# Optimization experiments

Hardware: AMD Instinct MI355X
Metric: run time of the kernel (lower is better)

The kernel has to match this reference:

```python
import jax, jax.numpy as jnp
import numpy as np

L = 64            # max_l (spherical harmonic bandlimit)
NLAT = L          # latitude samples (Gauss-Legendre nodes)
NLON = 2 * L - 1  # longitude samples
C_IN = 64
C_OUT = 64
T_EMB = 128


def _legendre(Lmax, x):
    """Normalized associated Legendre Pbar_lm(x) (spherical-harmonic norm,
    Condon-Shortley phase) for m>=0. Returns (Lmax, Lmax, nlat)."""
    sx = np.sqrt(np.maximum(1.0 - x * x, 0.0))
    P = np.zeros((Lmax, Lmax, x.size))
    P[0, 0] = np.sqrt(1.0 / (4.0 * np.pi))
    for m in range(1, Lmax):
        P[m, m] = -np.sqrt((2 * m + 1) / (2.0 * m)) * sx * P[m - 1, m - 1]
    for m in range(Lmax - 1):
        P[m + 1, m] = np.sqrt(2 * m + 3.0) * x * P[m, m]
    for m in range(Lmax):
        for l in range(m + 2, Lmax):
            a = np.sqrt((4.0 * l * l - 1.0) / (l * l - m * m))
            b = np.sqrt(((l - 1.0) ** 2 - m * m) / (4.0 * (l - 1.0) ** 2 - 1.0))
            P[l, m] = a * (x * P[l - 1, m] - b * P[l - 2, m])
    return P


def _sht_matrices():
    # Gauss-Legendre quadrature in cos(theta): exact SHT for bandlimited signals
    xg, wg = np.polynomial.legendre.leggauss(NLAT)
    P = _legendre(L, xg)
    # extend to negative m: Pbar_{l,-m} = (-1)^m Pbar_{l,m}; m index offset L-1 (s2fft layout)
    Pfull = np.zeros((L, 2 * L - 1, NLAT))
    Pfull[:, L - 1] = P[:, 0]
    for m in range(1, L):
        Pfull[:, L - 1 + m] = P[:, m]
        Pfull[:, L - 1 - m] = ((-1) ** m) * P[:, m]
    m_idx = np.arange(-(L - 1), L) % NLON  # FFT bin for each m (bijective since NLON=2L-1)
    return jnp.asarray(Pfull, jnp.float32), jnp.asarray(wg, jnp.float32), m_idx


def setup_inputs():
    key = jax.random.key(0)
    k = jax.random.split(key, 6)
    w_std = np.float32(np.sqrt(1.0 / (2.0 * C_IN)))   # normal_initializer(in_channels)
    d_std = np.float32(np.sqrt(1.0 / T_EMB))          # flax Dense lecun_normal stddev
    n_spec = L * (2 * L - 1) * C_IN
    return {
        "x": jax.random.normal(k[0], (NLAT, NLON, C_IN), jnp.float32),
        "t_emb": jax.random.normal(k[1], (T_EMB,), jnp.float32),
        "weights_real": w_std * jax.random.normal(k[2], (L, C_IN, C_OUT), jnp.float32),
        "weights_imag": w_std * jax.random.normal(k[3], (L, C_IN, C_OUT), jnp.float32),
        "dense_w_real": d_std * jax.random.normal(k[4], (T_EMB, n_spec), jnp.float32),
        "dense_w_imag": d_std * jax.random.normal(k[5], (T_EMB, n_spec), jnp.float32),
    }


def reference(x, t_emb, weights_real, weights_imag, dense_w_real, dense_w_imag):
    Pfull, wg, m_idx = _sht_matrices()
    # ---- forward SHT (all channels at once): FFT over longitude + Legendre quadrature
    fm = jnp.fft.fft(x.astype(jnp.complex64), axis=1)[:, m_idx, :] * (2.0 * np.pi / NLON)  # (nlat, 2L-1, Cin)
    PW = (Pfull * wg[None, None, :]).astype(jnp.complex64)           # (L, 2L-1, nlat)
    x_sht = jnp.einsum('lmt,tmc->lmc', PW, fm)                        # (L, 2L-1, Cin)
    # ---- per-degree spectral conv
    weights = weights_real + 1j * weights_imag                        # (L, Cin, Cout)
    conv = jnp.einsum('lmi,lio->lmo', x_sht, weights)                 # (L, 2L-1, Cout)
    # ---- time-embedding injection (complex Dense without bias)
    t_c = (t_emb @ dense_w_real + 1j * (t_emb @ dense_w_imag)).reshape(L, 2 * L - 1, C_IN)
    result = t_c + conv
    # ---- inverse SHT
    fm_out = jnp.einsum('lmc,lmt->tmc', result, Pfull.astype(jnp.complex64))  # (nlat, 2L-1, Cout)
    g = jnp.zeros((NLAT, NLON, C_OUT), jnp.complex64).at[:, m_idx, :].set(fm_out)
    out = jnp.fft.ifft(g, axis=1) * NLON                              # (nlat, nlon, Cout)
    return jnp.transpose(out, (2, 0, 1))  # (Cout, nlat, nlon), complex64 (matches vmap out_axes=0)
```

## Files before the change

kernel.cpp:

```cpp
#include <hip/hip_runtime.h>
#include <hip/hip_bf16.h>
#include <math.h>
#include <stdint.h>

#define NLAT 64
#define NLON 127
#define LMAX 64
#define CCH  64
#define TEMB 128
#define ROW  (NLON * CCH)
#define PLANE (LMAX * NLON * CCH)
#define NEEDED_WS (1024 + 5ull * PLANE * 4ull)

static __device__ __constant__ double PI_D = 3.14159265358979323846;
#define TWO_PI_127F 0.049473784494768665f

__global__ void k_band(float band, __hip_bfloat16* __restrict__ out) {
    int n = blockIdx.x, t = blockIdx.y, c = threadIdx.x;
    __hip_bfloat162 v;
    v.x = __float2bfloat16(band);
    v.y = __float2bfloat16(band);
    ((__hip_bfloat162*)out)[((size_t)c * 64 + t) * 127 + n] = v;
}

__global__ void k_gauss(double* __restrict__ xg, float* __restrict__ wgf) {
    int i = threadIdx.x;
    if (i >= NLAT) return;
    const int n = 64;
    int k = 63 - i;
    double x = cos(PI_D * ((double)k + 0.75) / ((double)n + 0.5));
    for (int it = 0; it < 8; ++it) {
        double p0 = 1.0, p1 = x;
        for (int kk = 2; kk <= n; ++kk) {
            double p2 = ((2.0 * kk - 1.0) * x * p1 - (kk - 1.0) * p0) * (1.0 / kk);
            p0 = p1; p1 = p2;
        }
        double dpn = n * (x * p1 - p0) / (x * x - 1.0);
        x -= p1 / dpn;
    }
    double p0 = 1.0, p1 = x;
    for (int kk = 2; kk <= n; ++kk) {
        double p2 = ((2.0 * kk - 1.0) * x * p1 - (kk - 1.0) * p0) * (1.0 / kk);
        p0 = p1; p1 = p2;
    }
    double dpn = n * (x * p1 - p0) / (x * x - 1.0);
    xg[i] = x;
    wgf[i] = (float)(2.0 / ((1.0 - x * x) * dpn * dpn));
}

__global__ void k_legendre(const double* __restrict__ xg, float* __restrict__ Pf) {
    int m = blockIdx.x;
    int t = threadIdx.x;
    double x = xg[t];
    double sx = sqrt(fmax(1.0 - x * x, 0.0));
    double pmm = sqrt(1.0 / (4.0 * PI_D));
    for (int k = 1; k <= m; ++k)
        pmm *= -sqrt((2.0 * k + 1.0) / (2.0 * k)) * sx;
    float sgn = (m & 1) ? -1.0f : 1.0f;
    int jp = (63 + m) * 4096;
    int jn = (63 - m) * 4096;
    for (int l = 0; l < m; ++l) {
        Pf[jp + l * 64 + t] = 0.0f;
        if (m) Pf[jn + l * 64 + t] = 0.0f;
    }
    Pf[jp + m * 64 + t] = (float)pmm;
    if (m) Pf[jn + m * 64 + t] = sgn * (float)pmm;
    if (m + 1 < LMAX) {
        double plm2 = pmm;
        double plm1 = sqrt(2.0 * m + 3.0) * x * pmm;
        Pf[jp + (m + 1) * 64 + t] = (float)plm1;
        if (m) Pf[jn + (m + 1) * 64 + t] = sgn * (float)plm1;
        for (int l = m + 2; l < LMAX; ++l) {
            double a = sqrt((4.0 * (double)l * l - 1.0) / ((double)l * l - (double)m * m));
            double lm1 = (double)(l - 1);
            double b = sqrt((lm1 * lm1 - (double)m * m) / (4.0 * lm1 * lm1 - 1.0));
            double pl = a * (x * plm1 - b * plm2);
            Pf[jp + l * 64 + t] = (float)pl;
            if (m) Pf[jn + l * 64 + t] = sgn * (float)pl;
            plm2 = plm1; plm1 = pl;
        }
    }
}

__global__ __launch_bounds__(256) void k_dft_fwd(const float* __restrict__ x,
                                                 float* __restrict__ fmr,
                                                 float* __restrict__ fmi) {
    __shared__ float xs[NLON * CCH];
    __shared__ float ctab[NLON], stab[NLON];
    int t = blockIdx.x;
    int jbase = blockIdx.y * 32;
    int tid = threadIdx.x;
    for (int idx = tid; idx < NLON * CCH; idx += 256)
        xs[idx] = x[t * ROW + idx];
    if (tid < NLON) {
        double th = 2.0 * PI_D * (double)tid / 127.0;
        ctab[tid] = (float)cos(th);
        stab[tid] = (float)sin(th);
    }
    __syncthreads();
    int c = tid & 63;
    int jl = tid >> 6;
    float ar[8], ai[8];
    int p[8], mm[8];
#pragma unroll
    for (int q = 0; q < 8; ++q) {
        ar[q] = 0.f; ai[q] = 0.f; p[q] = 0;
        int j = jbase + jl + 4 * q;
        int m = j - 63;
        mm[q] = (j <= 126) ? (m < 0 ? m + 127 : m) : 0;
    }
    for (int n = 0; n < NLON; ++n) {
        float xv = xs[n * 64 + c];
#pragma unroll
        for (int q = 0; q < 8; ++q) {
            ar[q] = fmaf(xv, ctab[p[q]], ar[q]);
            ai[q] = fmaf(-xv, stab[p[q]], ai[q]);
            p[q] += mm[q]; if (p[q] >= 127) p[q] -= 127;
        }
    }
#pragma unroll
    for (int q = 0; q < 8; ++q) {
        int j = jbase + jl + 4 * q;
        if (j <= 126) {
            fmr[t * ROW + j * 64 + c] = ar[q] * TWO_PI_127F;
            fmi[t * ROW + j * 64 + c] = ai[q] * TWO_PI_127F;
        }
    }
}

__global__ __launch_bounds__(256) void k_sht(const float* __restrict__ Pf,
                                             const float* __restrict__ wgf,
                                             const float* __restrict__ fmr,
                                             const float* __restrict__ fmi,
                                             float* __restrict__ xsr,
                                             float* __restrict__ xsi) {
    __shared__ float Pw[LMAX * NLAT];
    __shared__ float fr[NLAT * CCH], fi[NLAT * CCH];
    int j = blockIdx.x;
    int tid = threadIdx.x;
    for (int idx = tid; idx < LMAX * NLAT; idx += 256)
        Pw[idx] = Pf[j * 4096 + idx] * wgf[idx & 63];
    for (int idx = tid; idx < NLAT * CCH; idx += 256) {
        int t = idx >> 6;
        fr[idx] = fmr[t * ROW + j * 64 + (idx & 63)];
        fi[idx] = fmi[t * ROW + j * 64 + (idx & 63)];
    }
    __syncthreads();
    int c = tid & 63, lb = tid >> 6;
    float ar[16] = {}, ai[16] = {};
    for (int t = 0; t < NLAT; ++t) {
        float frv = fr[t * 64 + c], fiv = fi[t * 64 + c];
#pragma unroll
        for (int q = 0; q < 16; ++q) {
            float pv = Pw[(lb + 4 * q) * 64 + t];
            ar[q] = fmaf(pv, frv, ar[q]);
            ai[q] = fmaf(pv, fiv, ai[q]);
        }
    }
#pragma unroll
    for (int q = 0; q < 16; ++q) {
        int l = lb + 4 * q;
        xsr[l * ROW + j * 64 + c] = ar[q];
        xsi[l * ROW + j * 64 + c] = ai[q];
    }
}

__global__ __launch_bounds__(256) void k_conv(const float* __restrict__ xsr,
                                              const float* __restrict__ xsi,
                                              const float* __restrict__ Wr,
                                              const float* __restrict__ Wi,
                                              float* __restrict__ cvr,
                                              float* __restrict__ cvi) {
    __shared__ float xr[64 * 64], xi[64 * 64];
    __shared__ float wr[64 * 64], wi[64 * 64];
    int l = blockIdx.x;
    int jbase = blockIdx.y * 64;
    int tid = threadIdx.x;
    for (int idx = tid; idx < 4096; idx += 256) {
        int jl = idx >> 6, i = idx & 63;
        int j = jbase + jl;
        bool ok = (j < NLON);
        xr[idx] = ok ? xsr[l * ROW + j * 64 + i] : 0.f;
        xi[idx] = ok ? xsi[l * ROW + j * 64 + i] : 0.f;
        wr[idx] = Wr[l * 4096 + idx];
        wi[idx] = Wi[l * 4096 + idx];
    }
    __syncthreads();
    int o = tid & 63, jb = tid >> 6;
    float ar[16] = {}, ai[16] = {};
    for (int i = 0; i < 64; ++i) {
        float wrv = wr[i * 64 + o], wiv = wi[i * 64 + o];
#pragma unroll
        for (int q = 0; q < 16; ++q) {
            float xrv = xr[(jb + 4 * q) * 64 + i];
            float xiv = xi[(jb + 4 * q) * 64 + i];
            ar[q] = fmaf(xrv, wrv, fmaf(-xiv, wiv, ar[q]));
            ai[q] = fmaf(xrv, wiv, fmaf(xiv, wrv, ai[q]));
        }
    }
#pragma unroll
    for (int q = 0; q < 16; ++q) {
        int j = jbase + jb + 4 * q;
        if (j < NLON) {
            cvr[l * ROW + j * 64 + o] = ar[q];
            cvi[l * ROW + j * 64 + o] = ai[q];
        }
    }
}

__global__ __launch_bounds__(256) void k_dense(const float* __restrict__ temb,
                                               const float* __restrict__ dwr,
                                               const float* __restrict__ dwi,
                                               const float* __restrict__ cvr,
                                               const float* __restrict__ cvi,
                                               float* __restrict__ rsr,
                                               float* __restrict__ rsi) {
    __shared__ float te[TEMB];
    int tid = threadIdx.x;
    if (tid < TEMB) te[tid] = temb[tid];
    __syncthreads();
    size_t s2 = (size_t)blockIdx.x * 256 + tid;
    const float2* wr2 = (const float2*)dwr;
    const float2* wi2 = (const float2*)dwi;
    float2 ar = {0, 0}, ai = {0, 0};
#pragma unroll 16
    for (int k = 0; k < TEMB; ++k) {
        float tk = te[k];
        float2 a = wr2[(size_t)k * (PLANE / 2) + s2];
        float2 b = wi2[(size_t)k * (PLANE / 2) + s2];
        ar.x = fmaf(tk, a.x, ar.x); ar.y = fmaf(tk, a.y, ar.y);
        ai.x = fmaf(tk, b.x, ai.x); ai.y = fmaf(tk, b.y, ai.y);
    }
    float2 cr = ((const float2*)cvr)[s2];
    float2 ci = ((const float2*)cvi)[s2];
    ar.x += cr.x; ar.y += cr.y;
    ai.x += ci.x; ai.y += ci.y;
    ((float2*)rsr)[s2] = ar;
    ((float2*)rsi)[s2] = ai;
}

__global__ __launch_bounds__(256) void k_isht(const float* __restrict__ Pf,
                                              const float* __restrict__ rsr,
                                              const float* __restrict__ rsi,
                                              float* __restrict__ fo_r,
                                              float* __restrict__ fo_i) {
    __shared__ float Pl[LMAX * NLAT];
    __shared__ float rr[LMAX * CCH], ri[LMAX * CCH];
    int j = blockIdx.x;
    int tid = threadIdx.x;
    for (int idx = tid; idx < LMAX * NLAT; idx += 256)
        Pl[idx] = Pf[j * 4096 + idx];
    for (int idx = tid; idx < LMAX * CCH; idx += 256) {
        int l = idx >> 6;
        rr[idx] = rsr[l * ROW + j * 64 + (idx & 63)];
        ri[idx] = rsi[l * ROW + j * 64 + (idx & 63)];
    }
    __syncthreads();
    int c = tid & 63, tb = tid >> 6;
    float ar[16] = {}, ai[16] = {};
    for (int l = 0; l < LMAX; ++l) {
        float rv = rr[l * 64 + c], iv = ri[l * 64 + c];
#pragma unroll
        for (int q = 0; q < 16; ++q) {
            float pv = Pl[l * 64 + (tb + 4 * q)];
            ar[q] = fmaf(pv, rv, ar[q]);
            ai[q] = fmaf(pv, iv, ai[q]);
        }
    }
#pragma unroll
    for (int q = 0; q < 16; ++q) {
        int t = tb + 4 * q;
        fo_r[t * ROW + j * 64 + c] = ar[q];
        fo_i[t * ROW + j * 64 + c] = ai[q];
    }
}

__global__ __launch_bounds__(256) void k_idft(const float* __restrict__ fo_r,
                                              const float* __restrict__ fo_i,
                                              __hip_bfloat16* __restrict__ out) {
    __shared__ float fr[NLON * CCH], fi[NLON * CCH];
    __shared__ float ctab[NLON], stab[NLON];
    int t = blockIdx.x;
    int nbase = blockIdx.y * 64;
    int tid = threadIdx.x;
    for (int idx = tid; idx < NLON * CCH; idx += 256) {
        fr[idx] = fo_r[t * ROW + idx];
        fi[idx] = fo_i[t * ROW + idx];
    }
    if (tid < NLON) {
        double th = 2.0 * PI_D * (double)tid / 127.0;
        ctab[tid] = (float)cos(th);
        stab[tid] = (float)sin(th);
    }
    __syncthreads();
    int nl = tid & 63, cb = tid >> 6;
    int n = nbase + nl;
    bool act = (n < NLON);
    int step = act ? n : 0;
    int p = act ? (64 * n) % 127 : 0;
    float ar[16] = {}, ai[16] = {};
    for (int jj = 0; jj < NLON; ++jj) {
        float cv = ctab[p], sv = stab[p];
#pragma unroll
        for (int q = 0; q < 16; ++q) {
            float frv = fr[jj * 64 + cb + 4 * q];
            float fiv = fi[jj * 64 + cb + 4 * q];
            ar[q] = fmaf(frv, cv, fmaf(-fiv, sv, ar[q]));
            ai[q] = fmaf(frv, sv, fmaf(fiv, cv, ai[q]));
        }
        p += step; if (p >= 127) p -= 127;
    }
    if (act) {
#pragma unroll
        for (int q = 0; q < 16; ++q) {
            int cc = cb + 4 * q;
            size_t pp = ((size_t)cc * 64 + t) * 127 + n;
            out[2 * pp + 1] = __float2bfloat16(ar[q]);
            if (pp + 1 < (size_t)PLANE)
                out[2 * pp + 2] = __float2bfloat16(ai[q]);
            if (pp == 0)
                out[0] = __float2bfloat16(0.0f);
        }
    }
}

static inline bool rng_overlap(uintptr_t a0, uintptr_t a1, uintptr_t b0, uintptr_t b1) {
    return (a0 < b1) && (b0 < a1);
}

extern "C" void kernel_launch(void* const* d_in, const int* in_sizes, int n_in,
                              void* d_out, int out_size, void* d_ws, size_t ws_size,
                              hipStream_t stream) {
    const float* x    = (const float*)d_in[0];
    const float* temb = (const float*)d_in[1];
    const float* Wr   = (const float*)d_in[2];
    const float* Wi   = (const float*)d_in[3];
    const float* dwr  = (const float*)d_in[4];
    const float* dwi  = (const float*)d_in[5];

    __hip_bfloat16* out = (__hip_bfloat16*)d_out;
    dim3 g2(127, 64);

    if (d_ws == nullptr || ws_size < NEEDED_WS) {
        size_t mb = ws_size >> 20;
        if (mb > 60) mb = 60;
        k_band<<<g2, 64, 0, stream>>>(20000.0f + 256.0f * (float)mb, out);
        return;
    }
    int bits = 0;
    {
        bool ok = (n_in >= 6) && (in_sizes[0] == 520192) && (in_sizes[1] == 128) &&
                  (in_sizes[2] == 262144) && (in_sizes[3] == 262144) &&
                  (in_sizes[4] == 66584576) && (in_sizes[5] == 66584576);
        if (!ok) bits |= 1;
    }
    uintptr_t w0 = (uintptr_t)d_ws, w1 = w0 + NEEDED_WS;
    uintptr_t o0 = (uintptr_t)d_out, o1 = o0 + (size_t)out_size * 2;
    if (rng_overlap(w0, w1, o0, o1)) bits |= 4;
    for (int i = 0; i < n_in && i < 6; ++i) {
        uintptr_t b0 = (uintptr_t)d_in[i];
        uintptr_t b1 = b0 + (size_t)in_sizes[i] * 4;
        if (rng_overlap(w0, w1, b0, b1)) bits |= 8;
    }
    if (bits) {
        k_band<<<g2, 64, 0, stream>>>(3000.0f + 400.0f * (float)bits, out);
        return;
    }

    char* ws = (char*)d_ws;
    double* xg = (double*)ws;
    float* wgf = (float*)(ws + 512);
    size_t off = 1024;
    float* Pf = (float*)(ws + off); off += (size_t)PLANE * 4;
    float* Ar = (float*)(ws + off); off += (size_t)PLANE * 4;
    float* Ai = (float*)(ws + off); off += (size_t)PLANE * 4;
    float* Br = (float*)(ws + off); off += (size_t)PLANE * 4;
    float* Bi = (float*)(ws + off);

    k_gauss   <<<1, 64, 0, stream>>>(xg, wgf);
    k_legendre<<<64, 64, 0, stream>>>(xg, Pf);
    k_dft_fwd <<<dim3(64, 4), 256, 0, stream>>>(x, Ar, Ai);
    k_sht     <<<127, 256, 0, stream>>>(Pf, wgf, Ar, Ai, Br, Bi);
    k_conv    <<<dim3(64, 2), 256, 0, stream>>>(Br, Bi, Wr, Wi, Ar, Ai);
    k_dense   <<<PLANE / 512, 256, 0, stream>>>(temb, dwr, dwi, Ar, Ai, Br, Bi);
    k_isht    <<<127, 256, 0, stream>>>(Pf, Br, Bi, Ar, Ai);
    k_idft    <<<dim3(64, 2), 256, 0, stream>>>(Ar, Ai, out);
}
```

Baseline: 253.8 us.

## Split SHT, conv, ISHT and IDFT grids in half and batch dense loads

Halves the per-block work in k_sht, k_conv, k_isht and k_idft by adding a grid dimension over degree, longitude or latitude halves, doubling the block count so more of the GPU's compute units are busy. Each thread now keeps 8 accumulators instead of 16, which lowers register pressure. k_dense is restructured to issue eight pairs of weight loads per iteration before the FMAs, giving more memory-level parallelism on the large dense-weight stream. The cost is redundant loading of the shared fm/rs/weight tiles across the split blocks.

```diff
diff --git a/kernel.cpp b/kernel.cpp
--- a/kernel.cpp
+++ b/kernel.cpp
@@ -134,32 +134,35 @@
                                              const float* __restrict__ fmi,
                                              float* __restrict__ xsr,
                                              float* __restrict__ xsi) {
-    __shared__ float Pw[LMAX * NLAT];
+    __shared__ float Pw[32 * NLAT];
     __shared__ float fr[NLAT * CCH], fi[NLAT * CCH];
     int j = blockIdx.x;
-    int tid = threadIdx.x;
-    for (int idx = tid; idx < LMAX * NLAT; idx += 256)
-        Pw[idx] = Pf[j * 4096 + idx] * wgf[idx & 63];
+    int half = blockIdx.y;
+    int tid = threadIdx.x;
+    for (int idx = tid; idx < 32 * NLAT; idx += 256) {
+        int ll = idx >> 6, t = idx & 63;
+        Pw[idx] = Pf[j * 4096 + (half * 32 + ll) * 64 + t] * wgf[t];
+    }
     for (int idx = tid; idx < NLAT * CCH; idx += 256) {
         int t = idx >> 6;
         fr[idx] = fmr[t * ROW + j * 64 + (idx & 63)];
         fi[idx] = fmi[t * ROW + j * 64 + (idx & 63)];
     }
     __syncthreads();
-    int c = tid & 63, lb = tid >> 6;
-    float ar[16] = {}, ai[16] = {};
+    int c = tid & 63, lg = tid >> 6;
+    float ar[8] = {}, ai[8] = {};
     for (int t = 0; t < NLAT; ++t) {
         float frv = fr[t * 64 + c], fiv = fi[t * 64 + c];
 #pragma unroll
-        for (int q = 0; q < 16; ++q) {
-            float pv = Pw[(lb + 4 * q) * 64 + t];
+        for (int q = 0; q < 8; ++q) {
+            float pv = Pw[(lg + 4 * q) * 64 + t];
             ar[q] = fmaf(pv, frv, ar[q]);
             ai[q] = fmaf(pv, fiv, ai[q]);
         }
     }
 #pragma unroll
-    for (int q = 0; q < 16; ++q) {
-        int l = lb + 4 * q;
+    for (int q = 0; q < 8; ++q) {
+        int l = half * 32 + lg + 4 * q;
         xsr[l * ROW + j * 64 + c] = ar[q];
         xsi[l * ROW + j * 64 + c] = ai[q];
     }
@@ -171,27 +174,29 @@
                                               const float* __restrict__ Wi,
                                               float* __restrict__ cvr,
                                               float* __restrict__ cvi) {
-    __shared__ float xr[64 * 64], xi[64 * 64];
+    __shared__ float xr[32 * 64], xi[32 * 64];
     __shared__ float wr[64 * 64], wi[64 * 64];
     int l = blockIdx.x;
-    int jbase = blockIdx.y * 64;
-    int tid = threadIdx.x;
-    for (int idx = tid; idx < 4096; idx += 256) {
+    int jbase = blockIdx.y * 32;
+    int tid = threadIdx.x;
+    for (int idx = tid; idx < 2048; idx += 256) {
         int jl = idx >> 6, i = idx & 63;
         int j = jbase + jl;
         bool ok = (j < NLON);
         xr[idx] = ok ? xsr[l * ROW + j * 64 + i] : 0.f;
         xi[idx] = ok ? xsi[l * ROW + j * 64 + i] : 0.f;
+    }
+    for (int idx = tid; idx < 4096; idx += 256) {
         wr[idx] = Wr[l * 4096 + idx];
         wi[idx] = Wi[l * 4096 + idx];
     }
     __syncthreads();
     int o = tid & 63, jb = tid >> 6;
-    float ar[16] = {}, ai[16] = {};
+    float ar[8] = {}, ai[8] = {};
     for (int i = 0; i < 64; ++i) {
         float wrv = wr[i * 64 + o], wiv = wi[i * 64 + o];
 #pragma unroll
-        for (int q = 0; q < 16; ++q) {
+        for (int q = 0; q < 8; ++q) {
             float xrv = xr[(jb + 4 * q) * 64 + i];
             float xiv = xi[(jb + 4 * q) * 64 + i];
             ar[q] = fmaf(xrv, wrv, fmaf(-xiv, wiv, ar[q]));
@@ -199,7 +204,7 @@
         }
     }
 #pragma unroll
-    for (int q = 0; q < 16; ++q) {
+    for (int q = 0; q < 8; ++q) {
         int j = jbase + jb + 4 * q;
         if (j < NLON) {
             cvr[l * ROW + j * 64 + o] = ar[q];
@@ -223,13 +228,37 @@
     const float2* wr2 = (const float2*)dwr;
     const float2* wi2 = (const float2*)dwi;
     float2 ar = {0, 0}, ai = {0, 0};
-#pragma unroll 16
-    for (int k = 0; k < TEMB; ++k) {
-        float tk = te[k];
-        float2 a = wr2[(size_t)k * (PLANE / 2) + s2];
-        float2 b = wi2[(size_t)k * (PLANE / 2) + s2];
-        ar.x = fmaf(tk, a.x, ar.x); ar.y = fmaf(tk, a.y, ar.y);
-        ai.x = fmaf(tk, b.x, ai.x); ai.y = fmaf(tk, b.y, ai.y);
+    for (int kk = 0; kk < TEMB; kk += 8) {
+        float2 a0, a1, a2, a3, a4, a5, a6, a7;
+        float2 b0, b1, b2, b3, b4, b5, b6, b7;
+        const float2* pr = wr2 + (size_t)kk * (PLANE / 2) + s2;
+        const float2* pi = wi2 + (size_t)kk * (PLANE / 2) + s2;
+        a0 = pr[0 * (PLANE / 2)]; b0 = pi[0 * (PLANE / 2)];
+        a1 = pr[1 * (PLANE / 2)]; b1 = pi[1 * (PLANE / 2)];
+        a2 = pr[2 * (PLANE / 2)]; b2 = pi[2 * (PLANE / 2)];
+        a3 = pr[3 * (PLANE / 2)]; b3 = pi[3 * (PLANE / 2)];
+        a4 = pr[4 * (PLANE / 2)]; b4 = pi[4 * (PLANE / 2)];
+        a5 = pr[5 * (PLANE / 2)]; b5 = pi[5 * (PLANE / 2)];
+        a6 = pr[6 * (PLANE / 2)]; b6 = pi[6 * (PLANE / 2)];
+        a7 = pr[7 * (PLANE / 2)]; b7 = pi[7 * (PLANE / 2)];
+        float t0 = te[kk], t1 = te[kk + 1], t2 = te[kk + 2], t3 = te[kk + 3];
+        float t4 = te[kk + 4], t5 = te[kk + 5], t6 = te[kk + 6], t7 = te[kk + 7];
+        ar.x = fmaf(t0, a0.x, ar.x); ar.y = fmaf(t0, a0.y, ar.y);
+        ai.x = fmaf(t0, b0.x, ai.x); ai.y = fmaf(t0, b0.y, ai.y);
+        ar.x = fmaf(t1, a1.x, ar.x); ar.y = fmaf(t1, a1.y, ar.y);
+        ai.x = fmaf(t1, b1.x, ai.x); ai.y = fmaf(t1, b1.y, ai.y);
+        ar.x = fmaf(t2, a2.x, ar.x); ar.y = fmaf(t2, a2.y, ar.y);
+        ai.x = fmaf(t2, b2.x, ai.x); ai.y = fmaf(t2, b2.y, ai.y);
+        ar.x = fmaf(t3, a3.x, ar.x); ar.y = fmaf(t3, a3.y, ar.y);
+        ai.x = fmaf(t3, b3.x, ai.x); ai.y = fmaf(t3, b3.y, ai.y);
+        ar.x = fmaf(t4, a4.x, ar.x); ar.y = fmaf(t4, a4.y, ar.y);
+        ai.x = fmaf(t4, b4.x, ai.x); ai.y = fmaf(t4, b4.y, ai.y);
+        ar.x = fmaf(t5, a5.x, ar.x); ar.y = fmaf(t5, a5.y, ar.y);
+        ai.x = fmaf(t5, b5.x, ai.x); ai.y = fmaf(t5, b5.y, ai.y);
+        ar.x = fmaf(t6, a6.x, ar.x); ar.y = fmaf(t6, a6.y, ar.y);
+        ai.x = fmaf(t6, b6.x, ai.x); ai.y = fmaf(t6, b6.y, ai.y);
+        ar.x = fmaf(t7, a7.x, ar.x); ar.y = fmaf(t7, a7.y, ar.y);
+        ai.x = fmaf(t7, b7.x, ai.x); ai.y = fmaf(t7, b7.y, ai.y);
     }
     float2 cr = ((const float2*)cvr)[s2];
     float2 ci = ((const float2*)cvi)[s2];
@@ -244,12 +273,15 @@
                                               const float* __restrict__ rsi,
                                               float* __restrict__ fo_r,
                                               float* __restrict__ fo_i) {
-    __shared__ float Pl[LMAX * NLAT];
+    __shared__ float Pl[LMAX * 32];
     __shared__ float rr[LMAX * CCH], ri[LMAX * CCH];
     int j = blockIdx.x;
-    int tid = threadIdx.x;
-    for (int idx = tid; idx < LMAX * NLAT; idx += 256)
-        Pl[idx] = Pf[j * 4096 + idx];
+    int half = blockIdx.y;
+    int tid = threadIdx.x;
+    for (int idx = tid; idx < LMAX * 32; idx += 256) {
+        int l = idx >> 5, tloc = idx & 31;
+        Pl[idx] = Pf[j * 4096 + l * 64 + (half * 32 + tloc)];
+    }
     for (int idx = tid; idx < LMAX * CCH; idx += 256) {
         int l = idx >> 6;
         rr[idx] = rsr[l * ROW + j * 64 + (idx & 63)];
@@ -257,19 +289,19 @@
     }
     __syncthreads();
     int c = tid & 63, tb = tid >> 6;
-    float ar[16] = {}, ai[16] = {};
+    float ar[8] = {}, ai[8] = {};
     for (int l = 0; l < LMAX; ++l) {
         float rv = rr[l * 64 + c], iv = ri[l * 64 + c];
 #pragma unroll
-        for (int q = 0; q < 16; ++q) {
-            float pv = Pl[l * 64 + (tb + 4 * q)];
+        for (int q = 0; q < 8; ++q) {
+            float pv = Pl[l * 32 + (tb + 4 * q)];
             ar[q] = fmaf(pv, rv, ar[q]);
             ai[q] = fmaf(pv, iv, ai[q]);
         }
     }
 #pragma unroll
-    for (int q = 0; q < 16; ++q) {
-        int t = tb + 4 * q;
+    for (int q = 0; q < 8; ++q) {
+        int t = half * 32 + tb + 4 * q;
         fo_r[t * ROW + j * 64 + c] = ar[q];
         fo_i[t * ROW + j * 64 + c] = ai[q];
     }
@@ -281,7 +313,7 @@
     __shared__ float fr[NLON * CCH], fi[NLON * CCH];
     __shared__ float ctab[NLON], stab[NLON];
     int t = blockIdx.x;
-    int nbase = blockIdx.y * 64;
+    int nbase = blockIdx.y * 32;
     int tid = threadIdx.x;
     for (int idx = tid; idx < NLON * CCH; idx += 256) {
         fr[idx] = fo_r[t * ROW + idx];
@@ -293,18 +325,18 @@
         stab[tid] = (float)sin(th);
     }
     __syncthreads();
-    int nl = tid & 63, cb = tid >> 6;
+    int nl = tid & 31, cg = tid >> 5;
     int n = nbase + nl;
     bool act = (n < NLON);
     int step = act ? n : 0;
     int p = act ? (64 * n) % 127 : 0;
-    float ar[16] = {}, ai[16] = {};
+    float ar[8] = {}, ai[8] = {};
     for (int jj = 0; jj < NLON; ++jj) {
         float cv = ctab[p], sv = stab[p];
 #pragma unroll
-        for (int q = 0; q < 16; ++q) {
-            float frv = fr[jj * 64 + cb + 4 * q];
-            float fiv = fi[jj * 64 + cb + 4 * q];
+        for (int q = 0; q < 8; ++q) {
+            float frv = fr[jj * 64 + cg + 8 * q];
+            float fiv = fi[jj * 64 + cg + 8 * q];
             ar[q] = fmaf(frv, cv, fmaf(-fiv, sv, ar[q]));
             ai[q] = fmaf(frv, sv, fmaf(fiv, cv, ai[q]));
         }
@@ -312,8 +344,8 @@
     }
     if (act) {
 #pragma unroll
-        for (int q = 0; q < 16; ++q) {
-            int cc = cb + 4 * q;
+        for (int q = 0; q < 8; ++q) {
+            int cc = cg + 8 * q;
             size_t pp = ((size_t)cc * 64 + t) * 127 + n;
             out[2 * pp + 1] = __float2bfloat16(ar[q]);
             if (pp + 1 < (size_t)PLANE)
@@ -380,9 +412,9 @@
     k_gauss   <<<1, 64, 0, stream>>>(xg, wgf);
     k_legendre<<<64, 64, 0, stream>>>(xg, Pf);
     k_dft_fwd <<<dim3(64, 4), 256, 0, stream>>>(x, Ar, Ai);
-    k_sht     <<<127, 256, 0, stream>>>(Pf, wgf, Ar, Ai, Br, Bi);
-    k_conv    <<<dim3(64, 2), 256, 0, stream>>>(Br, Bi, Wr, Wi, Ar, Ai);
+    k_sht     <<<dim3(127, 2), 256, 0, stream>>>(Pf, wgf, Ar, Ai, Br, Bi);
+    k_conv    <<<dim3(64, 4), 256, 0, stream>>>(Br, Bi, Wr, Wi, Ar, Ai);
     k_dense   <<<PLANE / 512, 256, 0, stream>>>(temb, dwr, dwi, Ar, Ai, Br, Bi);
-    k_isht    <<<127, 256, 0, stream>>>(Pf, Br, Bi, Ar, Ai);
-    k_idft    <<<dim3(64, 2), 256, 0, stream>>>(Ar, Ai, out);
-}
+    k_isht    <<<dim3(127, 2), 256, 0, stream>>>(Pf, Br, Bi, Ar, Ai);
+    k_idft    <<<dim3(64, 4), 256, 0, stream>>>(Ar, Ai, out);
+}
```

Measured after the change: 230.3 us. 9.3% less time.
